# Kernel tuning notes

Hardware: AMD Instinct MI355X
Metric: run time of the kernel (lower is better)

The kernel has to match this reference:

```python
import jax, jax.numpy as jnp
import numpy as np

N = 100000      # nodes
E = 625000      # edges
F_IN = 128      # num_features
C = 32          # num_classes


def setup_inputs() -> dict:
    key = jax.random.key(0)
    k1, k2, k3, k4, k5 = jax.random.split(key, 5)
    x = jax.random.normal(k1, (N, F_IN), dtype=jnp.float32)
    edge_index = jax.random.randint(k2, (2, E), 0, N, dtype=jnp.int64)
    s = 1.0 / np.sqrt(F_IN)
    # PyG SAGEConv: lin_l (applied to aggregated neighbors, with bias), lin_r (applied to self, no bias)
    W_l = jax.random.uniform(k3, (C, F_IN), dtype=jnp.float32, minval=-s, maxval=s)
    b_l = jax.random.uniform(k4, (C,), dtype=jnp.float32, minval=-s, maxval=s)
    W_r = jax.random.uniform(k5, (C, F_IN), dtype=jnp.float32, minval=-s, maxval=s)
    return {"x": x, "edge_index": edge_index, "W_l": W_l, "b_l": b_l, "W_r": W_r}


def reference(x, edge_index, W_l, b_l, W_r):
    src, dst = edge_index[0], edge_index[1]
    # mean aggregation of source-node features at destination nodes
    msg_sum = jax.ops.segment_sum(x[src], dst, num_segments=N)            # [N, F]
    deg = jax.ops.segment_sum(jnp.ones((E,), x.dtype), dst, num_segments=N)
    agg = msg_sum / jnp.maximum(deg, 1.0)[:, None]
    # SAGEConv: lin_l(agg) + lin_r(x)
    h = agg @ W_l.T + b_l + x @ W_r.T                                     # [N, C]
    h = jax.nn.relu(h)
    # dropout is identity in eval mode
    return jax.nn.log_softmax(h, axis=1)
```

## Files before the change

### kernel.cpp

```cpp
#include <hip/hip_runtime.h>
#include <math.h>

#define F_IN 128
#define NCLS 32
#define ZC   64
#define CAP  64
#define NPART 8
#define PADW 136

typedef __attribute__((ext_vector_type(8))) short short8v;
typedef __attribute__((ext_vector_type(4))) float f32x4;

__device__ __forceinline__ unsigned int pk2(float lo, float hi) {
    unsigned int a = __float_as_uint(lo), b = __float_as_uint(hi);
    a = (a + 0x7fffu + ((a >> 16) & 1u)) >> 16;
    b = (b + 0x7fffu + ((b >> 16) & 1u)) >> 16;
    return a | (b << 16);
}
__device__ __forceinline__ uint4 pack8(float4 a, float4 b) {
    return make_uint4(pk2(a.x, a.y), pk2(a.z, a.w), pk2(b.x, b.y), pk2(b.z, b.w));
}

__global__ __launch_bounds__(256) void proj_kernel(const float* __restrict__ x,
                                                   const float* __restrict__ Wl,
                                                   const float* __restrict__ Wr,
                                                   float* __restrict__ z,
                                                   int* __restrict__ cnt, int N) {
    __shared__ __align__(16) unsigned short xs[64 * PADW];
    __shared__ __align__(16) unsigned short ws[64 * PADW];
    int t = threadIdx.x;
    int node0 = blockIdx.x * 64;

    if (t < 64) {
        int n = node0 + t;
        if (n < N) cnt[n] = 0;
    }

    #pragma unroll
    for (int p = 0; p < 4; ++p) {
        int idx = t + p * 256;
        int row = idx >> 4;
        int q   = idx & 15;
        const float* srcW = (row < NCLS) ? (Wl + row * F_IN) : (Wr + (row - NCLS) * F_IN);
        float4 wa = *(const float4*)(srcW + q * 8);
        float4 wb = *(const float4*)(srcW + q * 8 + 4);
        *(uint4*)(ws + row * PADW + q * 8) = pack8(wa, wb);

        int node = node0 + row;
        int safe = (node < N) ? node : (N - 1);
        const float* srcX = x + (size_t)safe * F_IN;
        float4 xa = *(const float4*)(srcX + q * 8);
        float4 xb = *(const float4*)(srcX + q * 8 + 4);
        *(uint4*)(xs + row * PADW + q * 8) = pack8(xa, xb);
    }
    __syncthreads();

    int wave = t >> 6;
    int lane = t & 63;
    int l15  = lane & 15;
    int koff = (lane >> 4) * 8;

    f32x4 acc[4] = {{0.f,0.f,0.f,0.f},{0.f,0.f,0.f,0.f},{0.f,0.f,0.f,0.f},{0.f,0.f,0.f,0.f}};
    const unsigned short* xrow = xs + (wave * 16 + l15) * PADW + koff;
    const unsigned short* wrow = ws + l15 * PADW + koff;

    #pragma unroll
    for (int ks = 0; ks < 4; ++ks) {
        short8v a = *reinterpret_cast<const short8v*>(xrow + ks * 32);
        #pragma unroll
        for (int ct = 0; ct < 4; ++ct) {
            short8v b = *reinterpret_cast<const short8v*>(wrow + ct * 16 * PADW + ks * 32);
            acc[ct] = __builtin_amdgcn_mfma_f32_16x16x32_bf16(a, b, acc[ct], 0, 0, 0);
        }
    }

    int r0 = (lane >> 4) * 4;
    #pragma unroll
    for (int ct = 0; ct < 4; ++ct) {
        #pragma unroll
        for (int r = 0; r < 4; ++r) {
            int node = node0 + wave * 16 + r0 + r;
            if (node < N) z[(size_t)node * ZC + ct * 16 + l15] = acc[ct][r];
        }
    }
}

__global__ __launch_bounds__(256) void fill_kernel(const void* __restrict__ ei,
                                                   int* __restrict__ cnt,
                                                   int* __restrict__ col,
                                                   int E, int N, int span) {
    const unsigned int* u = (const unsigned int*)ei;
    unsigned int a = 0;
    #pragma unroll
    for (int j = 0; j < 16; ++j) a |= u[2 * j + 1];
    int is64 = (a == 0u);

    int part = blockIdx.x & (NPART - 1);
    int e0 = ((blockIdx.x >> 3) * 256 + threadIdx.x) * 4;
    if (e0 >= E) return;
    int lo = part * span;
    int hi = lo + span; if (hi > N) hi = N;
    int ecnt = (E - e0 >= 4) ? 4 : (E - e0);

    int d[4];
    if (is64) {
        const long long* dp = (const long long*)ei + E + e0;
        if (ecnt == 4) {
            longlong2 d01 = *(const longlong2*)dp, d23 = *(const longlong2*)(dp + 2);
            d[0]=(int)d01.x; d[1]=(int)d01.y; d[2]=(int)d23.x; d[3]=(int)d23.y;
        } else {
            for (int j = 0; j < ecnt; ++j) d[j] = (int)dp[j];
        }
    } else {
        const int* dp = (const int*)ei + E + e0;
        if (ecnt == 4) {
            int4 dv = *(const int4*)dp;
            d[0]=dv.x; d[1]=dv.y; d[2]=dv.z; d[3]=dv.w;
        } else {
            for (int j = 0; j < ecnt; ++j) d[j] = dp[j];
        }
    }

    for (int j = 0; j < ecnt; ++j) {
        if (d[j] >= lo && d[j] < hi) {
            int sv = is64 ? (int)((const long long*)ei)[e0 + j]
                          : ((const int*)ei)[e0 + j];
            if ((unsigned)sv >= (unsigned)N) sv = 0;
            int pos = atomicAdd(&cnt[d[j]], 1);
            if (pos < CAP) col[(size_t)d[j] * CAP + pos] = sv;
        }
    }
}

__global__ __launch_bounds__(256) void finish_kernel(const float* __restrict__ z,
                                                     const int* __restrict__ col,
                                                     const int* __restrict__ cnt,
                                                     const float* __restrict__ bl,
                                                     float* __restrict__ out, int N) {
    int gid = blockIdx.x * 256 + threadIdx.x;
    int node = gid >> 5;
    int c = gid & 31;
    if (node >= N) return;

    int deg = cnt[node];
    int m = (deg < CAP) ? deg : CAP;
    const int* cb = col + (size_t)node * CAP;
    float selfz = z[(size_t)node * ZC + NCLS + c];
    float bias  = bl[c];

    float a[8] = {};
    for (int base = 0; base < m; base += 8) {
        int4 n0 = *(const int4*)(cb + base);
        int4 n1 = *(const int4*)(cb + base + 4);
        int idx[8] = {n0.x, n0.y, n0.z, n0.w, n1.x, n1.y, n1.z, n1.w};
        #pragma unroll
        for (int k = 0; k < 8; ++k) {
            bool ok = (base + k < m);
            int s = ok ? idx[k] : 0;
            float v = z[(size_t)s * ZC + c];
            a[k] += ok ? v : 0.f;
        }
    }
    float acc = ((a[0] + a[1]) + (a[2] + a[3])) + ((a[4] + a[5]) + (a[6] + a[7]));

    float inv = 1.0f / fmaxf((float)deg, 1.0f);
    float h = acc * inv + bias + selfz;
    h = fmaxf(h, 0.f);

    float mx = h;
    #pragma unroll
    for (int o = 16; o >= 1; o >>= 1) mx = fmaxf(mx, __shfl_xor(mx, o));
    float p = h - mx;
    float ex = __expf(p);
    float s = ex;
    #pragma unroll
    for (int o = 16; o >= 1; o >>= 1) s += __shfl_xor(s, o);

    out[(size_t)node * NCLS + c] = p - __logf(s);
}

__global__ void detect_i64_kernel(const unsigned int* __restrict__ ei, int* __restrict__ flag) {
    if (blockIdx.x == 0 && threadIdx.x == 0) {
        unsigned int acc = 0;
        #pragma unroll
        for (int i = 0; i < 64; ++i) acc |= ei[2 * i + 1];
        *flag = (acc == 0u) ? 1 : 0;
    }
}

__global__ __launch_bounds__(256) void scatter_kernel(const float* __restrict__ x,
                                                      const void* __restrict__ ei,
                                                      const int* __restrict__ flag,
                                                      float* __restrict__ msg,
                                                      float* __restrict__ deg, int E, int N) {
    long long gid = (long long)blockIdx.x * blockDim.x + threadIdx.x;
    int e = (int)(gid >> 5);
    if (e >= E) return;
    int c = (int)(gid & 31);
    int is64 = *flag;
    int src = is64 ? (int)((const long long*)ei)[e] : ((const int*)ei)[e];
    int dst = is64 ? (int)((const long long*)ei)[(size_t)E + e] : ((const int*)ei)[(size_t)E + e];
    if ((unsigned)src >= (unsigned)N || (unsigned)dst >= (unsigned)N) return;
    float4 v = *(const float4*)(x + (size_t)src * F_IN + (c << 2));
    float* m = msg + (size_t)dst * F_IN + (c << 2);
    atomicAdd(m + 0, v.x);
    atomicAdd(m + 1, v.y);
    atomicAdd(m + 2, v.z);
    atomicAdd(m + 3, v.w);
    if (c == 0) atomicAdd(deg + dst, 1.0f);
}

__global__ __launch_bounds__(256) void apply_kernel(const float* __restrict__ x,
                                                    const float* __restrict__ msg,
                                                    const float* __restrict__ degf,
                                                    const float* __restrict__ Wl,
                                                    const float* __restrict__ bl,
                                                    const float* __restrict__ Wr,
                                                    float* __restrict__ out, int N) {
    int n = blockIdx.x * 256 + threadIdx.x;
    if (n >= N) return;
    float inv = 1.0f / fmaxf(degf[n], 1.0f);
    float acc[NCLS];
    #pragma unroll
    for (int c = 0; c < NCLS; ++c) acc[c] = bl[c];
    const float* xr = x + (size_t)n * F_IN;
    const float* mr = msg + (size_t)n * F_IN;
    for (int kb = 0; kb < F_IN; kb += 4) {
        float4 xv = *(const float4*)(xr + kb);
        float4 mv = *(const float4*)(mr + kb);
        float b0 = mv.x * inv, b1 = mv.y * inv, b2 = mv.z * inv, b3 = mv.w * inv;
        #pragma unroll
        for (int c = 0; c < NCLS; ++c) {
            float4 wl = *(const float4*)(Wl + c * F_IN + kb);
            float4 wr = *(const float4*)(Wr + c * F_IN + kb);
            acc[c] += b0 * wl.x + b1 * wl.y + b2 * wl.z + b3 * wl.w
                    + xv.x * wr.x + xv.y * wr.y + xv.z * wr.z + xv.w * wr.w;
        }
    }
    float mx = 0.0f;
    #pragma unroll
    for (int c = 0; c < NCLS; ++c) { acc[c] = fmaxf(acc[c], 0.0f); mx = fmaxf(mx, acc[c]); }
    float s = 0.0f;
    #pragma unroll
    for (int c = 0; c < NCLS; ++c) s += __expf(acc[c] - mx);
    float lg = __logf(s);
    float* o = out + (size_t)n * NCLS;
    #pragma unroll
    for (int q = 0; q < NCLS; q += 4) {
        float4 w = make_float4(acc[q] - mx - lg, acc[q + 1] - mx - lg,
                               acc[q + 2] - mx - lg, acc[q + 3] - mx - lg);
        *(float4*)(o + q) = w;
    }
}

extern "C" void kernel_launch(void* const* d_in, const int* in_sizes, int n_in,
                              void* d_out, int out_size, void* d_ws, size_t ws_size,
                              hipStream_t stream) {
    const float* x  = (const float*)d_in[0];
    const void*  ei = d_in[1];
    const float* Wl = (const float*)d_in[2];
    const float* bl = (const float*)d_in[3];
    const float* Wr = (const float*)d_in[4];

    int N = in_sizes[0] / F_IN;
    int E = in_sizes[1] / 2;
    int span = (N + NPART - 1) / NPART;

    size_t need = ((size_t)N * ZC + (size_t)N + (size_t)N * CAP) * 4;

    if (ws_size >= need) {
        float* z   = (float*)d_ws;
        int*   cnt = (int*)(z + (size_t)N * ZC);
        int*   col = cnt + N;

        proj_kernel<<<(N + 63) / 64, 256, 0, stream>>>(x, Wl, Wr, z, cnt, N);

        int eb4 = (E + 1023) / 1024;
        fill_kernel<<<eb4 * NPART, 256, 0, stream>>>(ei, cnt, col, E, N, span);

        long long tot = (long long)N * 32;
        finish_kernel<<<(int)((tot + 255) / 256), 256, 0, stream>>>(z, col, cnt, bl,
                                                                    (float*)d_out, N);
    } else {
        float* msg  = (float*)d_ws;
        float* deg  = msg + (size_t)N * F_IN;
        int*   flag = (int*)(deg + N);

        hipMemsetAsync(d_ws, 0, ((size_t)N * F_IN + N) * 4, stream);
        detect_i64_kernel<<<1, 64, 0, stream>>>((const unsigned int*)ei, flag);

        long long tot = (long long)E * 32;
        scatter_kernel<<<(int)((tot + 255) / 256), 256, 0, stream>>>(x, ei, flag, msg, deg, E, N);
        apply_kernel<<<(N + 255) / 256, 256, 0, stream>>>(x, msg, deg, Wl, bl, Wr,
                                                          (float*)d_out, N);
    }
}
```

Baseline: 69.85 us.

## Fuse projection, CSR fill and finish into one cooperative persistent kernel

Replaces the three launches (projection, bucketed adjacency fill, gather+log-softmax) with a single cooperative kernel. It zeroes counts, syncs the grid, runs projection tiles and fill units in one phase, syncs the grid again, then runs the finish groups. This removes two kernel launch gaps and lets projection and fill overlap in one phase. In exchange it adds grid-wide barriers, host occupancy queries on every call, and grid-stride loops over a grid capped at 2048 blocks. The old kernels remain as a fallback.

Measured after the change: 202.5 us. 190% more time.

```diff
diff --git a/kernel.cpp b/kernel.cpp
--- a/kernel.cpp
+++ b/kernel.cpp
@@ -1,5 +1,8 @@
 #include <hip/hip_runtime.h>
+#include <hip/hip_cooperative_groups.h>
 #include <math.h>
+
+namespace cg = cooperative_groups;
 
 #define F_IN 128
 #define NCLS 32
@@ -19,6 +22,184 @@
 }
 __device__ __forceinline__ uint4 pack8(float4 a, float4 b) {
     return make_uint4(pk2(a.x, a.y), pk2(a.z, a.w), pk2(b.x, b.y), pk2(b.z, b.w));
+}
+
+__device__ __forceinline__ void dev_proj_tile(const float* __restrict__ x,
+                                              const float* __restrict__ Wl,
+                                              const float* __restrict__ Wr,
+                                              float* __restrict__ z, int N, int node0,
+                                              unsigned short* xs, unsigned short* ws, int t) {
+    __syncthreads();
+    #pragma unroll
+    for (int p = 0; p < 4; ++p) {
+        int idx = t + p * 256;
+        int row = idx >> 4;
+        int q   = idx & 15;
+        const float* srcW = (row < NCLS) ? (Wl + row * F_IN) : (Wr + (row - NCLS) * F_IN);
+        float4 wa = *(const float4*)(srcW + q * 8);
+        float4 wb = *(const float4*)(srcW + q * 8 + 4);
+        *(uint4*)(ws + row * PADW + q * 8) = pack8(wa, wb);
+
+        int node = node0 + row;
+        int safe = (node < N) ? node : (N - 1);
+        const float* srcX = x + (size_t)safe * F_IN;
+        float4 xa = *(const float4*)(srcX + q * 8);
+        float4 xb = *(const float4*)(srcX + q * 8 + 4);
+        *(uint4*)(xs + row * PADW + q * 8) = pack8(xa, xb);
+    }
+    __syncthreads();
+
+    int wave = t >> 6;
+    int lane = t & 63;
+    int l15  = lane & 15;
+    int koff = (lane >> 4) * 8;
+
+    f32x4 acc[4] = {{0.f,0.f,0.f,0.f},{0.f,0.f,0.f,0.f},{0.f,0.f,0.f,0.f},{0.f,0.f,0.f,0.f}};
+    const unsigned short* xrow = xs + (wave * 16 + l15) * PADW + koff;
+    const unsigned short* wrow = ws + l15 * PADW + koff;
+
+    #pragma unroll
+    for (int ks = 0; ks < 4; ++ks) {
+        short8v a = *reinterpret_cast<const short8v*>(xrow + ks * 32);
+        #pragma unroll
+        for (int ct = 0; ct < 4; ++ct) {
+            short8v bfr = *reinterpret_cast<const short8v*>(wrow + ct * 16 * PADW + ks * 32);
+            acc[ct] = __builtin_amdgcn_mfma_f32_16x16x32_bf16(a, bfr, acc[ct], 0, 0, 0);
+        }
+    }
+
+    int r0 = (lane >> 4) * 4;
+    #pragma unroll
+    for (int ct = 0; ct < 4; ++ct) {
+        #pragma unroll
+        for (int r = 0; r < 4; ++r) {
+            int node = node0 + wave * 16 + r0 + r;
+            if (node < N) z[(size_t)node * ZC + ct * 16 + l15] = acc[ct][r];
+        }
+    }
+}
+
+__device__ __forceinline__ void dev_fill_unit(const void* __restrict__ ei, int is64,
+                                              int* __restrict__ cnt, int* __restrict__ col,
+                                              int E, int N, int span, int u, int t) {
+    int part = u & (NPART - 1);
+    int e0 = ((u >> 3) * 256 + t) * 4;
+    if (e0 >= E) return;
+    int lo = part * span;
+    int hi = lo + span; if (hi > N) hi = N;
+    int ecnt = (E - e0 >= 4) ? 4 : (E - e0);
+
+    int d[4];
+    if (is64) {
+        const long long* dp = (const long long*)ei + E + e0;
+        if (ecnt == 4) {
+            longlong2 d01 = *(const longlong2*)dp, d23 = *(const longlong2*)(dp + 2);
+            d[0]=(int)d01.x; d[1]=(int)d01.y; d[2]=(int)d23.x; d[3]=(int)d23.y;
+        } else {
+            for (int j = 0; j < ecnt; ++j) d[j] = (int)dp[j];
+        }
+    } else {
+        const int* dp = (const int*)ei + E + e0;
+        if (ecnt == 4) {
+            int4 dv = *(const int4*)dp;
+            d[0]=dv.x; d[1]=dv.y; d[2]=dv.z; d[3]=dv.w;
+        } else {
+            for (int j = 0; j < ecnt; ++j) d[j] = dp[j];
+        }
+    }
+
+    for (int j = 0; j < ecnt; ++j) {
+        if (d[j] >= lo && d[j] < hi) {
+            int sv = is64 ? (int)((const long long*)ei)[e0 + j]
+                          : ((const int*)ei)[e0 + j];
+            if ((unsigned)sv >= (unsigned)N) sv = 0;
+            int pos = atomicAdd(&cnt[d[j]], 1);
+            if (pos < CAP) col[(size_t)d[j] * CAP + pos] = sv;
+        }
+    }
+}
+
+__device__ __forceinline__ void dev_finish_group(const float* __restrict__ z,
+                                                 const int* __restrict__ col,
+                                                 const int* __restrict__ cnt,
+                                                 const float* __restrict__ bl,
+                                                 float* __restrict__ out, int N, int g, int t) {
+    int node = g * 8 + (t >> 5);
+    int c = t & 31;
+    if (node >= N) return;
+
+    int deg = cnt[node];
+    int m = (deg < CAP) ? deg : CAP;
+    const int* cb = col + (size_t)node * CAP;
+    float selfz = z[(size_t)node * ZC + NCLS + c];
+    float bias  = bl[c];
+
+    float a[8] = {};
+    for (int base = 0; base < m; base += 8) {
+        int4 n0 = *(const int4*)(cb + base);
+        int4 n1 = *(const int4*)(cb + base + 4);
+        int idx[8] = {n0.x, n0.y, n0.z, n0.w, n1.x, n1.y, n1.z, n1.w};
+        #pragma unroll
+        for (int k = 0; k < 8; ++k) {
+            bool ok = (base + k < m);
+            int s = ok ? idx[k] : 0;
+            float v = z[(size_t)s * ZC + c];
+            a[k] += ok ? v : 0.f;
+        }
+    }
+    float acc = ((a[0] + a[1]) + (a[2] + a[3])) + ((a[4] + a[5]) + (a[6] + a[7]));
+
+    float inv = 1.0f / fmaxf((float)deg, 1.0f);
+    float h = acc * inv + bias + selfz;
+    h = fmaxf(h, 0.f);
+
+    float mx = h;
+    #pragma unroll
+    for (int o = 16; o >= 1; o >>= 1) mx = fmaxf(mx, __shfl_xor(mx, o));
+    float p = h - mx;
+    float ex = __expf(p);
+    float s = ex;
+    #pragma unroll
+    for (int o = 16; o >= 1; o >>= 1) s += __shfl_xor(s, o);
+
+    out[(size_t)node * NCLS + c] = p - __logf(s);
+}
+
+__global__ __launch_bounds__(256) void fused_kernel(const float* __restrict__ x,
+                                                    const void* __restrict__ ei,
+                                                    const float* __restrict__ Wl,
+                                                    const float* __restrict__ bl,
+                                                    const float* __restrict__ Wr,
+                                                    float* __restrict__ z,
+                                                    int* __restrict__ cnt,
+                                                    int* __restrict__ col,
+                                                    float* __restrict__ out,
+                                                    int N, int E, int span,
+                                                    int T, int FU, int G) {
+    __shared__ __align__(16) unsigned short xs[64 * PADW];
+    __shared__ __align__(16) unsigned short ws[64 * PADW];
+    int t = threadIdx.x;
+    int b = blockIdx.x;
+    int GB = gridDim.x;
+    cg::grid_group grid = cg::this_grid();
+
+    for (int i = b * 256 + t; i < N; i += GB * 256) cnt[i] = 0;
+    grid.sync();
+
+    for (int tile = b; tile < T; tile += GB)
+        dev_proj_tile(x, Wl, Wr, z, N, tile * 64, xs, ws, t);
+
+    const unsigned int* u32 = (const unsigned int*)ei;
+    unsigned int aa = 0;
+    #pragma unroll
+    for (int j = 0; j < 16; ++j) aa |= u32[2 * j + 1];
+    int is64 = (aa == 0u);
+    for (int u = b; u < FU; u += GB)
+        dev_fill_unit(ei, is64, cnt, col, E, N, span, u, t);
+    grid.sync();
+
+    for (int g = b; g < G; g += GB)
+        dev_finish_group(z, col, cnt, bl, out, N, g, t);
 }
 
 __global__ __launch_bounds__(256) void proj_kernel(const float* __restrict__ x,
@@ -30,106 +211,23 @@
     __shared__ __align__(16) unsigned short ws[64 * PADW];
     int t = threadIdx.x;
     int node0 = blockIdx.x * 64;
-
     if (t < 64) {
         int n = node0 + t;
         if (n < N) cnt[n] = 0;
     }
-
-    #pragma unroll
-    for (int p = 0; p < 4; ++p) {
-        int idx = t + p * 256;
-        int row = idx >> 4;
-        int q   = idx & 15;
-        const float* srcW = (row < NCLS) ? (Wl + row * F_IN) : (Wr + (row - NCLS) * F_IN);
-        float4 wa = *(const float4*)(srcW + q * 8);
-        float4 wb = *(const float4*)(srcW + q * 8 + 4);
-        *(uint4*)(ws + row * PADW + q * 8) = pack8(wa, wb);
-
-        int node = node0 + row;
-        int safe = (node < N) ? node : (N - 1);
-        const float* srcX = x + (size_t)safe * F_IN;
-        float4 xa = *(const float4*)(srcX + q * 8);
-        float4 xb = *(const float4*)(srcX + q * 8 + 4);
-        *(uint4*)(xs + row * PADW + q * 8) = pack8(xa, xb);
-    }
-    __syncthreads();
-
-    int wave = t >> 6;
-    int lane = t & 63;
-    int l15  = lane & 15;
-    int koff = (lane >> 4) * 8;
-
-    f32x4 acc[4] = {{0.f,0.f,0.f,0.f},{0.f,0.f,0.f,0.f},{0.f,0.f,0.f,0.f},{0.f,0.f,0.f,0.f}};
-    const unsigned short* xrow = xs + (wave * 16 + l15) * PADW + koff;
-    const unsigned short* wrow = ws + l15 * PADW + koff;
-
-    #pragma unroll
-    for (int ks = 0; ks < 4; ++ks) {
-        short8v a = *reinterpret_cast<const short8v*>(xrow + ks * 32);
-        #pragma unroll
-        for (int ct = 0; ct < 4; ++ct) {
-            short8v b = *reinterpret_cast<const short8v*>(wrow + ct * 16 * PADW + ks * 32);
-            acc[ct] = __builtin_amdgcn_mfma_f32_16x16x32_bf16(a, b, acc[ct], 0, 0, 0);
-        }
-    }
-
-    int r0 = (lane >> 4) * 4;
-    #pragma unroll
-    for (int ct = 0; ct < 4; ++ct) {
-        #pragma unroll
-        for (int r = 0; r < 4; ++r) {
-            int node = node0 + wave * 16 + r0 + r;
-            if (node < N) z[(size_t)node * ZC + ct * 16 + l15] = acc[ct][r];
-        }
-    }
+    dev_proj_tile(x, Wl, Wr, z, N, node0, xs, ws, t);
 }
 
 __global__ __launch_bounds__(256) void fill_kernel(const void* __restrict__ ei,
                                                    int* __restrict__ cnt,
                                                    int* __restrict__ col,
                                                    int E, int N, int span) {
-    const unsigned int* u = (const unsigned int*)ei;
+    const unsigned int* u32 = (const unsigned int*)ei;
     unsigned int a = 0;
     #pragma unroll
-    for (int j = 0; j < 16; ++j) a |= u[2 * j + 1];
+    for (int j = 0; j < 16; ++j) a |= u32[2 * j + 1];
     int is64 = (a == 0u);
-
-    int part = blockIdx.x & (NPART - 1);
-    int e0 = ((blockIdx.x >> 3) * 256 + threadIdx.x) * 4;
-    if (e0 >= E) return;
-    int lo = part * span;
-    int hi = lo + span; if (hi > N) hi = N;
-    int ecnt = (E - e0 >= 4) ? 4 : (E - e0);
-
-    int d[4];
-    if (is64) {
-        const long long* dp = (const long long*)ei + E + e0;
-        if (ecnt == 4) {
-            longlong2 d01 = *(const longlong2*)dp, d23 = *(const longlong2*)(dp + 2);
-            d[0]=(int)d01.x; d[1]=(int)d01.y; d[2]=(int)d23.x; d[3]=(int)d23.y;
-        } else {
-            for (int j = 0; j < ecnt; ++j) d[j] = (int)dp[j];
-        }
-    } else {
-        const int* dp = (const int*)ei + E + e0;
-        if (ecnt == 4) {
-            int4 dv = *(const int4*)dp;
-            d[0]=dv.x; d[1]=dv.y; d[2]=dv.z; d[3]=dv.w;
-        } else {
-            for (int j = 0; j < ecnt; ++j) d[j] = dp[j];
-        }
-    }
-
-    for (int j = 0; j < ecnt; ++j) {
-        if (d[j] >= lo && d[j] < hi) {
-            int sv = is64 ? (int)((const long long*)ei)[e0 + j]
-                          : ((const int*)ei)[e0 + j];
-            if ((unsigned)sv >= (unsigned)N) sv = 0;
-            int pos = atomicAdd(&cnt[d[j]], 1);
-            if (pos < CAP) col[(size_t)d[j] * CAP + pos] = sv;
-        }
-    }
+    dev_fill_unit(ei, is64, cnt, col, E, N, span, blockIdx.x, threadIdx.x);
 }
 
 __global__ __launch_bounds__(256) void finish_kernel(const float* __restrict__ z,
@@ -137,46 +235,7 @@
                                                      const int* __restrict__ cnt,
                                                      const float* __restrict__ bl,
                                                      float* __restrict__ out, int N) {
-    int gid = blockIdx.x * 256 + threadIdx.x;
-    int node = gid >> 5;
-    int c = gid & 31;
-    if (node >= N) return;
-
-    int deg = cnt[node];
-    int m = (deg < CAP) ? deg : CAP;
-    const int* cb = col + (size_t)node * CAP;
-    float selfz = z[(size_t)node * ZC + NCLS + c];
-    float bias  = bl[c];
-
-    float a[8] = {};
-    for (int base = 0; base < m; base += 8) {
-        int4 n0 = *(const int4*)(cb + base);
-        int4 n1 = *(const int4*)(cb + base + 4);
-        int idx[8] = {n0.x, n0.y, n0.z, n0.w, n1.x, n1.y, n1.z, n1.w};
-        #pragma unroll
-        for (int k = 0; k < 8; ++k) {
-            bool ok = (base + k < m);
-            int s = ok ? idx[k] : 0;
-            float v = z[(size_t)s * ZC + c];
-            a[k] += ok ? v : 0.f;
-        }
-    }
-    float acc = ((a[0] + a[1]) + (a[2] + a[3])) + ((a[4] + a[5]) + (a[6] + a[7]));
-
-    float inv = 1.0f / fmaxf((float)deg, 1.0f);
-    float h = acc * inv + bias + selfz;
-    h = fmaxf(h, 0.f);
-
-    float mx = h;
-    #pragma unroll
-    for (int o = 16; o >= 1; o >>= 1) mx = fmaxf(mx, __shfl_xor(mx, o));
-    float p = h - mx;
-    float ex = __expf(p);
-    float s = ex;
-    #pragma unroll
-    for (int o = 16; o >= 1; o >>= 1) s += __shfl_xor(s, o);
-
-    out[(size_t)node * NCLS + c] = p - __logf(s);
+    dev_finish_group(z, col, cnt, bl, out, N, blockIdx.x, threadIdx.x);
 }
 
 __global__ void detect_i64_kernel(const unsigned int* __restrict__ ei, int* __restrict__ flag) {
@@ -272,15 +331,43 @@
         float* z   = (float*)d_ws;
         int*   cnt = (int*)(z + (size_t)N * ZC);
         int*   col = cnt + N;
-
-        proj_kernel<<<(N + 63) / 64, 256, 0, stream>>>(x, Wl, Wr, z, cnt, N);
-
-        int eb4 = (E + 1023) / 1024;
-        fill_kernel<<<eb4 * NPART, 256, 0, stream>>>(ei, cnt, col, E, N, span);
-
-        long long tot = (long long)N * 32;
-        finish_kernel<<<(int)((tot + 255) / 256), 256, 0, stream>>>(z, col, cnt, bl,
-                                                                    (float*)d_out, N);
+        float* outp = (float*)d_out;
+
+        int T  = (N + 63) / 64;
+        int FU = ((E + 1023) / 1024) * NPART;
+        int G  = (N + 7) / 8;
+
+        int dev = 0;
+        hipGetDevice(&dev);
+        int numCU = 0;
+        hipDeviceGetAttribute(&numCU, hipDeviceAttributeMultiprocessorCount, dev);
+        int maxB = 0;
+        hipOccupancyMaxActiveBlocksPerMultiprocessor(&maxB, fused_kernel, 256, 0);
+
+        bool coop_ok = false;
+        if (numCU > 0 && maxB > 0) {
+            long long gb = (long long)numCU * maxB;
+            if (gb > 2048) gb = 2048;
+            gb &= ~7LL;
+            if (gb >= 8) {
+                int GB = (int)gb;
+                void* kargs[] = {(void*)&x, (void*)&ei, (void*)&Wl, (void*)&bl, (void*)&Wr,
+                                 (void*)&z, (void*)&cnt, (void*)&col, (void*)&outp,
+                                 (void*)&N, (void*)&E, (void*)&span,
+                                 (void*)&T, (void*)&FU, (void*)&G};
+                hipError_t err = hipLaunchCooperativeKernel((void*)fused_kernel,
+                                                            dim3(GB), dim3(256),
+                                                            kargs, 0, stream);
+                if (err == hipSuccess) coop_ok = true;
+                else (void)hipGetLastError();
+            }
+        }
+
+        if (!coop_ok) {
+            proj_kernel<<<T, 256, 0, stream>>>(x, Wl, Wr, z, cnt, N);
+            fill_kernel<<<FU, 256, 0, stream>>>(ei, cnt, col, E, N, span);
+            finish_kernel<<<G, 256, 0, stream>>>(z, col, cnt, bl, outp, N);
+        }
     } else {
         float* msg  = (float*)d_ws;
         float* deg  = msg + (size_t)N * F_IN;
```

## Merge projection and CSR fill into one launch; store projections as fp16

Applied to the files above, without the earlier changes.

The separate projection and edge-fill kernels become one grid: the first FU blocks do the bucketed edge fill and the remaining blocks do the MFMA projection, so the two independent phases can overlap on the GPU. Counter zeroing moves to a small zero_kernel launched first. The projected z buffer is now stored as fp16 instead of fp32, which halves the bytes of the random neighbour gathers in finish_kernel. The costs are an extra launch and fp16 rounding of the projection outputs.

Result: no change. 68.67 us (-1.7%).

```diff
diff --git a/kernel.cpp b/kernel.cpp
--- a/kernel.cpp
+++ b/kernel.cpp
@@ -1,4 +1,5 @@
 #include <hip/hip_runtime.h>
+#include <hip/hip_fp16.h>
 #include <math.h>
 
 #define F_IN 128
@@ -21,20 +22,75 @@
     return make_uint4(pk2(a.x, a.y), pk2(a.z, a.w), pk2(b.x, b.y), pk2(b.z, b.w));
 }
 
-__global__ __launch_bounds__(256) void proj_kernel(const float* __restrict__ x,
-                                                   const float* __restrict__ Wl,
-                                                   const float* __restrict__ Wr,
-                                                   float* __restrict__ z,
-                                                   int* __restrict__ cnt, int N) {
+__global__ __launch_bounds__(256) void zero_kernel(int* __restrict__ cnt, int N) {
+    int i = blockIdx.x * 256 + threadIdx.x;
+    if (i < N) cnt[i] = 0;
+}
+
+__device__ __forceinline__ void dev_fill_unit(const void* __restrict__ ei, int is64,
+                                              int* __restrict__ cnt, int* __restrict__ col,
+                                              int E, int N, int span, int u, int t) {
+    int part = u & (NPART - 1);
+    int e0 = ((u >> 3) * 256 + t) * 4;
+    if (e0 >= E) return;
+    int lo = part * span;
+    int hi = lo + span; if (hi > N) hi = N;
+    int ecnt = (E - e0 >= 4) ? 4 : (E - e0);
+
+    int d[4];
+    if (is64) {
+        const long long* dp = (const long long*)ei + E + e0;
+        if (ecnt == 4) {
+            longlong2 d01 = *(const longlong2*)dp, d23 = *(const longlong2*)(dp + 2);
+            d[0]=(int)d01.x; d[1]=(int)d01.y; d[2]=(int)d23.x; d[3]=(int)d23.y;
+        } else {
+            for (int j = 0; j < ecnt; ++j) d[j] = (int)dp[j];
+        }
+    } else {
+        const int* dp = (const int*)ei + E + e0;
+        if (ecnt == 4) {
+            int4 dv = *(const int4*)dp;
+            d[0]=dv.x; d[1]=dv.y; d[2]=dv.z; d[3]=dv.w;
+        } else {
+            for (int j = 0; j < ecnt; ++j) d[j] = dp[j];
+        }
+    }
+
+    for (int j = 0; j < ecnt; ++j) {
+        if (d[j] >= lo && d[j] < hi) {
+            int sv = is64 ? (int)((const long long*)ei)[e0 + j]
+                          : ((const int*)ei)[e0 + j];
+            if ((unsigned)sv >= (unsigned)N) sv = 0;
+            int pos = atomicAdd(&cnt[d[j]], 1);
+            if (pos < CAP) col[(size_t)d[j] * CAP + pos] = sv;
+        }
+    }
+}
+
+__global__ __launch_bounds__(256) void projfill_kernel(const float* __restrict__ x,
+                                                       const void* __restrict__ ei,
+                                                       const float* __restrict__ Wl,
+                                                       const float* __restrict__ Wr,
+                                                       __half* __restrict__ z,
+                                                       int* __restrict__ cnt,
+                                                       int* __restrict__ col,
+                                                       int N, int E, int span, int FU) {
     __shared__ __align__(16) unsigned short xs[64 * PADW];
     __shared__ __align__(16) unsigned short ws[64 * PADW];
     int t = threadIdx.x;
-    int node0 = blockIdx.x * 64;
-
-    if (t < 64) {
-        int n = node0 + t;
-        if (n < N) cnt[n] = 0;
-    }
+    int b = blockIdx.x;
+
+    if (b < FU) {
+        const unsigned int* u32 = (const unsigned int*)ei;
+        unsigned int aa = 0;
+        #pragma unroll
+        for (int j = 0; j < 16; ++j) aa |= u32[2 * j + 1];
+        int is64 = (aa == 0u);
+        dev_fill_unit(ei, is64, cnt, col, E, N, span, b, t);
+        return;
+    }
+
+    int node0 = (b - FU) * 64;
 
     #pragma unroll
     for (int p = 0; p < 4; ++p) {
@@ -69,8 +125,8 @@
         short8v a = *reinterpret_cast<const short8v*>(xrow + ks * 32);
         #pragma unroll
         for (int ct = 0; ct < 4; ++ct) {
-            short8v b = *reinterpret_cast<const short8v*>(wrow + ct * 16 * PADW + ks * 32);
-            acc[ct] = __builtin_amdgcn_mfma_f32_16x16x32_bf16(a, b, acc[ct], 0, 0, 0);
+            short8v bfr = *reinterpret_cast<const short8v*>(wrow + ct * 16 * PADW + ks * 32);
+            acc[ct] = __builtin_amdgcn_mfma_f32_16x16x32_bf16(a, bfr, acc[ct], 0, 0, 0);
         }
     }
 
@@ -80,59 +136,12 @@
         #pragma unroll
         for (int r = 0; r < 4; ++r) {
             int node = node0 + wave * 16 + r0 + r;
-            if (node < N) z[(size_t)node * ZC + ct * 16 + l15] = acc[ct][r];
-        }
-    }
-}
-
-__global__ __launch_bounds__(256) void fill_kernel(const void* __restrict__ ei,
-                                                   int* __restrict__ cnt,
-                                                   int* __restrict__ col,
-                                                   int E, int N, int span) {
-    const unsigned int* u = (const unsigned int*)ei;
-    unsigned int a = 0;
-    #pragma unroll
-    for (int j = 0; j < 16; ++j) a |= u[2 * j + 1];
-    int is64 = (a == 0u);
-
-    int part = blockIdx.x & (NPART - 1);
-    int e0 = ((blockIdx.x >> 3) * 256 + threadIdx.x) * 4;
-    if (e0 >= E) return;
-    int lo = part * span;
-    int hi = lo + span; if (hi > N) hi = N;
-    int ecnt = (E - e0 >= 4) ? 4 : (E - e0);
-
-    int d[4];
-    if (is64) {
-        const long long* dp = (const long long*)ei + E + e0;
-        if (ecnt == 4) {
-            longlong2 d01 = *(const longlong2*)dp, d23 = *(const longlong2*)(dp + 2);
-            d[0]=(int)d01.x; d[1]=(int)d01.y; d[2]=(int)d23.x; d[3]=(int)d23.y;
-        } else {
-            for (int j = 0; j < ecnt; ++j) d[j] = (int)dp[j];
-        }
-    } else {
-        const int* dp = (const int*)ei + E + e0;
-        if (ecnt == 4) {
-            int4 dv = *(const int4*)dp;
-            d[0]=dv.x; d[1]=dv.y; d[2]=dv.z; d[3]=dv.w;
-        } else {
-            for (int j = 0; j < ecnt; ++j) d[j] = dp[j];
-        }
-    }
-
-    for (int j = 0; j < ecnt; ++j) {
-        if (d[j] >= lo && d[j] < hi) {
-            int sv = is64 ? (int)((const long long*)ei)[e0 + j]
-                          : ((const int*)ei)[e0 + j];
-            if ((unsigned)sv >= (unsigned)N) sv = 0;
-            int pos = atomicAdd(&cnt[d[j]], 1);
-            if (pos < CAP) col[(size_t)d[j] * CAP + pos] = sv;
-        }
-    }
-}
-
-__global__ __launch_bounds__(256) void finish_kernel(const float* __restrict__ z,
+            if (node < N) z[(size_t)node * ZC + ct * 16 + l15] = __float2half(acc[ct][r]);
+        }
+    }
+}
+
+__global__ __launch_bounds__(256) void finish_kernel(const __half* __restrict__ z,
                                                      const int* __restrict__ col,
                                                      const int* __restrict__ cnt,
                                                      const float* __restrict__ bl,
@@ -145,7 +154,7 @@
     int deg = cnt[node];
     int m = (deg < CAP) ? deg : CAP;
     const int* cb = col + (size_t)node * CAP;
-    float selfz = z[(size_t)node * ZC + NCLS + c];
+    float selfz = __half2float(z[(size_t)node * ZC + NCLS + c]);
     float bias  = bl[c];
 
     float a[8] = {};
@@ -157,7 +166,7 @@
         for (int k = 0; k < 8; ++k) {
             bool ok = (base + k < m);
             int s = ok ? idx[k] : 0;
-            float v = z[(size_t)s * ZC + c];
+            float v = __half2float(z[(size_t)s * ZC + c]);
             a[k] += ok ? v : 0.f;
         }
     }
@@ -266,21 +275,23 @@
     int E = in_sizes[1] / 2;
     int span = (N + NPART - 1) / NPART;
 
-    size_t need = ((size_t)N * ZC + (size_t)N + (size_t)N * CAP) * 4;
+    size_t need = (size_t)N * ZC * 2 + (size_t)N * 4 + (size_t)N * CAP * 4;
 
     if (ws_size >= need) {
-        float* z   = (float*)d_ws;
-        int*   cnt = (int*)(z + (size_t)N * ZC);
-        int*   col = cnt + N;
-
-        proj_kernel<<<(N + 63) / 64, 256, 0, stream>>>(x, Wl, Wr, z, cnt, N);
-
-        int eb4 = (E + 1023) / 1024;
-        fill_kernel<<<eb4 * NPART, 256, 0, stream>>>(ei, cnt, col, E, N, span);
-
+        __half* z   = (__half*)d_ws;
+        int*    cnt = (int*)((char*)d_ws + (size_t)N * ZC * 2);
+        int*    col = cnt + N;
+        float*  outp = (float*)d_out;
+
+        int T  = (N + 63) / 64;
+        int FU = ((E + 1023) / 1024) * NPART;
+
+        zero_kernel<<<(N + 255) / 256, 256, 0, stream>>>(cnt, N);
+        projfill_kernel<<<FU + T, 256, 0, stream>>>(x, ei, Wl, Wr, z, cnt, col,
+                                                    N, E, span, FU);
         long long tot = (long long)N * 32;
         finish_kernel<<<(int)((tot + 255) / 256), 256, 0, stream>>>(z, col, cnt, bl,
-                                                                    (float*)d_out, N);
+                                                                    outp, N);
     } else {
         float* msg  = (float*)d_ws;
         float* deg  = msg + (size_t)N * F_IN;
```
